# Kernel optimization log

Measured on AMD Instinct MI355X. Metric: run time of the kernel, lower is better.

## Reference

```python
import jax, jax.numpy as jnp
import numpy as np

B, F, D = 512, 128, 1024
EPS = 1e-5

def _ln(x, g, b):
    mu = jnp.mean(x, axis=-1, keepdims=True)
    var = jnp.mean(jnp.square(x - mu), axis=-1, keepdims=True)
    return (x - mu) * jax.lax.rsqrt(var + EPS) * g + b

def setup_inputs() -> dict:
    key = jax.random.key(0)
    ks = jax.random.split(key, 8)
    inp = {
        "text_embeds": jax.random.normal(ks[0], (B, D), jnp.float32),
        "video_embeds": jax.random.normal(ks[1], (B, F, D), jnp.float32),
    }
    # Linear weights: torch init is eye for all proj/linear layers; use small random
    # perturbation of identity to keep math non-trivial but realistic.
    def w(k):
        return jnp.eye(D, dtype=jnp.float32) + 0.02 * jax.random.normal(k, (D, D), jnp.float32)
    inp["q_w"], inp["k_w"], inp["v_w"] = w(ks[2]), w(ks[3]), w(ks[4])
    inp["out_w"], inp["lin_w"] = w(ks[5]), w(ks[6])
    for n in ("q_b", "k_b", "v_b", "out_b", "lin_b"):
        inp[n] = jnp.zeros((D,), jnp.float32)
    for i in (1, 2, 3):
        inp[f"ln{i}_g"] = jnp.ones((D,), jnp.float32)
        inp[f"ln{i}_b"] = jnp.zeros((D,), jnp.float32)
    return inp

def reference(text_embeds, video_embeds, q_w, k_w, v_w, out_w, lin_w,
              q_b, k_b, v_b, out_b, lin_b,
              ln1_g, ln1_b, ln2_g, ln2_b, ln3_g, ln3_b):
    t = _ln(text_embeds, ln1_g, ln1_b)                 # [B, D]
    vf = _ln(video_embeds, ln1_g, ln1_b)               # [B, F, D]
    q = t @ q_w.T + q_b                                # [B, D]
    k = vf @ k_w.T + k_b                               # [B, F, D]
    v = vf @ v_w.T + v_b                               # [B, F, D]
    logits = jnp.einsum("bd,bfd->bf", q, k) / jnp.sqrt(jnp.float32(D))
    w_att = jax.nn.softmax(logits, axis=-1)            # [B, F]
    attn = jnp.einsum("bf,bfd->bd", w_att, v)          # [B, D]
    attn = attn @ out_w.T + out_b
    attn_out = _ln(attn, ln2_g, ln2_b)
    linear_out = attn_out @ lin_w.T + lin_b
    # dropout: eval mode (identity)
    out = attn_out + linear_out
    return _ln(out, ln3_g, ln3_b)
```

## Files before the change

### kernel.cpp

```cpp
#include <hip/hip_runtime.h>

#define B_ 512
#define F_ 128
#define D_ 1024
#define EPS_ 1e-5f

typedef float f32x4 __attribute__((ext_vector_type(4)));
typedef __bf16 bf16x4 __attribute__((ext_vector_type(4)));
typedef __bf16 bf16x8 __attribute__((ext_vector_type(8)));

template <int OUT>
__global__ __launch_bounds__(256) void k_ln(
    const float* __restrict__ X, const float* __restrict__ g,
    const float* __restrict__ bv, float* __restrict__ Yf,
    __bf16* __restrict__ Yh, __bf16* __restrict__ Yl) {
  int row = blockIdx.x, t = threadIdx.x;
  f32x4 xv = *(const f32x4*)(X + (size_t)row * D_ + t * 4);
  float s = xv[0] + xv[1] + xv[2] + xv[3];
  float ss = xv[0] * xv[0] + xv[1] * xv[1] + xv[2] * xv[2] + xv[3] * xv[3];
#pragma unroll
  for (int o = 32; o > 0; o >>= 1) { s += __shfl_xor(s, o); ss += __shfl_xor(ss, o); }
  __shared__ float ws[4][2];
  int w = t >> 6;
  if ((t & 63) == 0) { ws[w][0] = s; ws[w][1] = ss; }
  __syncthreads();
  s = ws[0][0] + ws[1][0] + ws[2][0] + ws[3][0];
  ss = ws[0][1] + ws[1][1] + ws[2][1] + ws[3][1];
  float mu = s * (1.0f / D_);
  float var = ss * (1.0f / D_) - mu * mu;
  float rs = rsqrtf(var + EPS_);
  f32x4 gg = *(const f32x4*)(g + t * 4);
  f32x4 bb = *(const f32x4*)(bv + t * 4);
  f32x4 o4;
#pragma unroll
  for (int i = 0; i < 4; i++) o4[i] = (xv[i] - mu) * rs * gg[i] + bb[i];
  if (OUT == 0) {
    *(f32x4*)(Yf + (size_t)row * D_ + t * 4) = o4;
  } else {
    bf16x4 h4, l4;
#pragma unroll
    for (int i = 0; i < 4; i++) {
      h4[i] = (__bf16)o4[i];
      l4[i] = (__bf16)(o4[i] - (float)h4[i]);
    }
    *(bf16x4*)(Yh + (size_t)row * D_ + t * 4) = h4;
    *(bf16x4*)(Yl + (size_t)row * D_ + t * 4) = l4;
  }
}

__global__ __launch_bounds__(256) void k_final(
    const __bf16* __restrict__ X1h, const __bf16* __restrict__ X1l,
    const float* __restrict__ X2, const float* __restrict__ g,
    const float* __restrict__ bv, float* __restrict__ out) {
  int row = blockIdx.x, t = threadIdx.x;
  bf16x4 h4 = *(const bf16x4*)(X1h + (size_t)row * D_ + t * 4);
  bf16x4 l4 = *(const bf16x4*)(X1l + (size_t)row * D_ + t * 4);
  f32x4 b = *(const f32x4*)(X2 + (size_t)row * D_ + t * 4);
  f32x4 v;
#pragma unroll
  for (int i = 0; i < 4; i++) v[i] = (float)h4[i] + (float)l4[i] + b[i];
  float s = v[0] + v[1] + v[2] + v[3];
  float ss = v[0] * v[0] + v[1] * v[1] + v[2] * v[2] + v[3] * v[3];
#pragma unroll
  for (int o = 32; o > 0; o >>= 1) { s += __shfl_xor(s, o); ss += __shfl_xor(ss, o); }
  __shared__ float ws[4][2];
  int w = t >> 6;
  if ((t & 63) == 0) { ws[w][0] = s; ws[w][1] = ss; }
  __syncthreads();
  s = ws[0][0] + ws[1][0] + ws[2][0] + ws[3][0];
  ss = ws[0][1] + ws[1][1] + ws[2][1] + ws[3][1];
  float mu = s * (1.0f / D_);
  float var = ss * (1.0f / D_) - mu * mu;
  float rs = rsqrtf(var + EPS_);
  f32x4 gg = *(const f32x4*)(g + t * 4);
  f32x4 bb = *(const f32x4*)(bv + t * 4);
  f32x4 o4;
#pragma unroll
  for (int i = 0; i < 4; i++) o4[i] = (v[i] - mu) * rs * gg[i] + bb[i];
  *(f32x4*)(out + (size_t)row * D_ + t * 4) = o4;
}

__global__ __launch_bounds__(256) void k_wprep(
    const float* __restrict__ w0, const float* __restrict__ w1,
    const float* __restrict__ w2, const float* __restrict__ w3,
    const float* __restrict__ w4, __bf16* __restrict__ o0,
    __bf16* __restrict__ o1, __bf16* __restrict__ o2,
    __bf16* __restrict__ o3, __bf16* __restrict__ o4p,
    const float* __restrict__ text, const float* __restrict__ g1,
    const float* __restrict__ b1, __bf16* __restrict__ Yh,
    __bf16* __restrict__ Yl) {
  int z = blockIdx.z;
  int t = threadIdx.x;
  if (z == 5) {
    int row = blockIdx.y * 32 + blockIdx.x;
    if (row >= B_) return;
    f32x4 xv = *(const f32x4*)(text + (size_t)row * D_ + t * 4);
    float s = xv[0] + xv[1] + xv[2] + xv[3];
    float ss = xv[0]*xv[0] + xv[1]*xv[1] + xv[2]*xv[2] + xv[3]*xv[3];
#pragma unroll
    for (int o = 32; o > 0; o >>= 1) { s += __shfl_xor(s, o); ss += __shfl_xor(ss, o); }
    __shared__ float ws[4][2];
    int w = t >> 6;
    if ((t & 63) == 0) { ws[w][0] = s; ws[w][1] = ss; }
    __syncthreads();
    s = ws[0][0] + ws[1][0] + ws[2][0] + ws[3][0];
    ss = ws[0][1] + ws[1][1] + ws[2][1] + ws[3][1];
    float mu = s * (1.0f / D_);
    float var = ss * (1.0f / D_) - mu * mu;
    float rs = rsqrtf(var + EPS_);
    f32x4 gg = *(const f32x4*)(g1 + t * 4);
    f32x4 bb = *(const f32x4*)(b1 + t * 4);
    bf16x4 h4, l4;
#pragma unroll
    for (int i = 0; i < 4; i++) {
      float o = (xv[i] - mu) * rs * gg[i] + bb[i];
      h4[i] = (__bf16)o;
      l4[i] = (__bf16)(o - (float)h4[i]);
    }
    *(bf16x4*)(Yh + (size_t)row * D_ + t * 4) = h4;
    *(bf16x4*)(Yl + (size_t)row * D_ + t * 4) = l4;
    return;
  }
  const float* src = (z == 0) ? w0 : (z == 1) ? w1 : (z == 2) ? w2 : (z == 3) ? w3 : w4;
  __bf16* dst = (z == 0) ? o0 : (z == 1) ? o1 : (z == 2) ? o2 : (z == 3) ? o3 : o4p;
  if (z != 1) {
    int row = blockIdx.y * 32 + (t >> 3);
    int col = blockIdx.x * 32 + (t & 7) * 4;
    f32x4 v = *(const f32x4*)(src + (size_t)row * D_ + col);
    bf16x4 o;
    o[0] = (__bf16)v[0]; o[1] = (__bf16)v[1]; o[2] = (__bf16)v[2]; o[3] = (__bf16)v[3];
    *(bf16x4*)(dst + (size_t)row * D_ + col) = o;
  } else {
    __shared__ float tile[32][33];
    int ti = blockIdx.y, tj = blockIdx.x;
    int c = t & 31, r0 = t >> 5;
#pragma unroll
    for (int i = 0; i < 4; i++) {
      int r = r0 + i * 8;
      tile[r][c] = src[(size_t)(ti * 32 + r) * D_ + tj * 32 + c];
    }
    __syncthreads();
#pragma unroll
    for (int i = 0; i < 4; i++) {
      int r = r0 + i * 8;
      dst[(size_t)(tj * 32 + r) * D_ + ti * 32 + c] = (__bf16)tile[c][r];
    }
  }
}

template <int OUT>
__global__ __launch_bounds__(512) void k_gemm32(
    const __bf16* __restrict__ Ah, const __bf16* __restrict__ Al,
    const __bf16* __restrict__ W, const float* __restrict__ bias,
    float* __restrict__ Cf, __bf16* __restrict__ Ch, __bf16* __restrict__ Cl,
    int N, int K) {
  int t = threadIdx.x;
  int lane = t & 63, wv = t >> 6;
  int r = lane & 15, quad = lane >> 4;
  int tn = blockIdx.x, tm = blockIdx.y;
  int kw = K >> 3;
  const __bf16* pah0 = Ah + (size_t)(tm * 32 + r) * K + wv * kw + quad * 8;
  const __bf16* pah1 = pah0 + (size_t)16 * K;
  const __bf16* pal0 = Al + (size_t)(tm * 32 + r) * K + wv * kw + quad * 8;
  const __bf16* pal1 = pal0 + (size_t)16 * K;
  const __bf16* pw0 = W + (size_t)(tn * 32 + r) * K + wv * kw + quad * 8;
  const __bf16* pw1 = pw0 + (size_t)16 * K;
  f32x4 acc00 = {0,0,0,0}, acc01 = {0,0,0,0}, acc10 = {0,0,0,0}, acc11 = {0,0,0,0};
  bf16x8 ah0 = *(const bf16x8*)pah0, ah1 = *(const bf16x8*)pah1;
  bf16x8 al0 = *(const bf16x8*)pal0, al1 = *(const bf16x8*)pal1;
  bf16x8 w0v = *(const bf16x8*)pw0, w1v = *(const bf16x8*)pw1;
  for (int k0 = 0; k0 < kw; k0 += 32) {
    int kn = (k0 + 32 < kw) ? (k0 + 32) : 0;
    bf16x8 nah0 = *(const bf16x8*)(pah0 + kn);
    bf16x8 nah1 = *(const bf16x8*)(pah1 + kn);
    bf16x8 nal0 = *(const bf16x8*)(pal0 + kn);
    bf16x8 nal1 = *(const bf16x8*)(pal1 + kn);
    bf16x8 nw0 = *(const bf16x8*)(pw0 + kn);
    bf16x8 nw1 = *(const bf16x8*)(pw1 + kn);
    acc00 = __builtin_amdgcn_mfma_f32_16x16x32_bf16(ah0, w0v, acc00, 0, 0, 0);
    acc01 = __builtin_amdgcn_mfma_f32_16x16x32_bf16(ah0, w1v, acc01, 0, 0, 0);
    acc10 = __builtin_amdgcn_mfma_f32_16x16x32_bf16(ah1, w0v, acc10, 0, 0, 0);
    acc11 = __builtin_amdgcn_mfma_f32_16x16x32_bf16(ah1, w1v, acc11, 0, 0, 0);
    acc00 = __builtin_amdgcn_mfma_f32_16x16x32_bf16(al0, w0v, acc00, 0, 0, 0);
    acc01 = __builtin_amdgcn_mfma_f32_16x16x32_bf16(al0, w1v, acc01, 0, 0, 0);
    acc10 = __builtin_amdgcn_mfma_f32_16x16x32_bf16(al1, w0v, acc10, 0, 0, 0);
    acc11 = __builtin_amdgcn_mfma_f32_16x16x32_bf16(al1, w1v, acc11, 0, 0, 0);
    ah0 = nah0; ah1 = nah1; al0 = nal0; al1 = nal1; w0v = nw0; w1v = nw1;
  }
  __shared__ float red[8][64][17];
  *(f32x4*)(&red[wv][lane][0])  = acc00;
  *(f32x4*)(&red[wv][lane][4])  = acc01;
  *(f32x4*)(&red[wv][lane][8])  = acc10;
  *(f32x4*)(&red[wv][lane][12]) = acc11;
  __syncthreads();
  int re = lane & 15, qe = lane >> 4;
#pragma unroll
  for (int u = 0; u < 2; u++) {
    int j = (t >> 6) * 2 + u;
    int a = j >> 2, i = j & 3;
    float val = 0.0f;
#pragma unroll
    for (int ww = 0; ww < 8; ww++) val += red[ww][lane][j];
    int row = tm * 32 + qe * 4 + i + ((a >> 1) << 4);
    int col = tn * 32 + re + ((a & 1) << 4);
    if (bias) val += bias[col];
    size_t o = (size_t)row * N + col;
    if (OUT == 0) {
      Cf[o] = val;
    } else {
      __bf16 h = (__bf16)val;
      Ch[o] = h;
      Cl[o] = (__bf16)(val - (float)h);
    }
  }
}

__global__ __launch_bounds__(1024) void k_attn(
    const float* __restrict__ video, const float* __restrict__ q2,
    const __bf16* __restrict__ qh, const __bf16* __restrict__ ql,
    const float* __restrict__ g, const float* __restrict__ bv,
    const float* __restrict__ kb, __bf16* __restrict__ ctxh,
    __bf16* __restrict__ ctxl) {
  __shared__ float Xc[16][1032];
  __shared__ float mSC[16][4];
  int b = blockIdx.x, t = threadIdx.x;
  int w = t >> 6, lane = t & 63;
  const float* vbase = video + ((size_t)b * F_ + w * 8) * D_ + lane * 4;
  f32x4 vA[4], vB[4];
#pragma unroll
  for (int i = 0; i < 4; i++) vA[i] = *(const f32x4*)(vbase + i * 256);
  const float* q2p = q2 + (size_t)b * D_ + lane * 4;
  const float* gp = g + lane * 4;
  const float* bp = bv + lane * 4;
  const float* kp = kb + lane * 4;
  const __bf16* qhp = qh + (size_t)b * D_ + lane * 4;
  const __bf16* qlp = ql + (size_t)b * D_ + lane * 4;
  f32x4 gqr[4];
  float s1 = 0.f, s2 = 0.f, s3 = 0.f;
#pragma unroll
  for (int i = 0; i < 4; i++) {
    f32x4 qv = *(const f32x4*)(q2p + i * 256);
    f32x4 g4 = *(const f32x4*)(gp + i * 256);
    f32x4 b4 = *(const f32x4*)(bp + i * 256);
    f32x4 k4 = *(const f32x4*)(kp + i * 256);
    bf16x4 h4 = *(const bf16x4*)(qhp + i * 256);
    bf16x4 l4 = *(const bf16x4*)(qlp + i * 256);
#pragma unroll
    for (int j = 0; j < 4; j++) {
      float gq = g4[j] * qv[j];
      gqr[i][j] = gq;
      s1 += gq;
      s2 += b4[j] * qv[j];
      s3 += k4[j] * ((float)h4[j] + (float)l4[j]);
    }
  }
#pragma unroll
  for (int o = 32; o > 0; o >>= 1) {
    s1 += __shfl_xor(s1, o); s2 += __shfl_xor(s2, o); s3 += __shfl_xor(s3, o);
  }
  float sgq = s1, dbq = s2, qk = s3;
  f32x4 O[4];
#pragma unroll
  for (int i = 0; i < 4; i++) O[i] = (f32x4){0.f, 0.f, 0.f, 0.f};
  float m_run = -1e30f, S = 0.0f, Cc = 0.0f;
  for (int f = 0; f < 8; f++) {
    if (f < 7) {
      const float* nb = vbase + (size_t)(f + 1) * D_;
#pragma unroll
      for (int i = 0; i < 4; i++) vB[i] = *(const f32x4*)(nb + i * 256);
    }
    float sx = 0.f, sxx = 0.f, sxg = 0.f;
#pragma unroll
    for (int i = 0; i < 4; i++) {
      f32x4 v = vA[i], gg = gqr[i];
#pragma unroll
      for (int j = 0; j < 4; j++) {
        sx += v[j];
        sxx += v[j] * v[j];
        sxg += v[j] * gg[j];
      }
    }
#pragma unroll
    for (int o = 32; o > 0; o >>= 1) {
      sx += __shfl_xor(sx, o);
      sxx += __shfl_xor(sxx, o);
      sxg += __shfl_xor(sxg, o);
    }
    float mu = sx * (1.0f / D_);
    float var = sxx * (1.0f / D_) - mu * mu;
    float rs = rsqrtf(var + EPS_);
    float l = (rs * (sxg - mu * sgq) + dbq + qk) * 0.03125f;
    float m_new = fmaxf(m_run, l);
    float alpha = __expf(m_run - m_new);
    float e = __expf(l - m_new);
    float af = e * rs;
    S = S * alpha + e;
    Cc = Cc * alpha + af * mu;
#pragma unroll
    for (int i = 0; i < 4; i++) {
#pragma unroll
      for (int j = 0; j < 4; j++) O[i][j] = O[i][j] * alpha + af * vA[i][j];
    }
    m_run = m_new;
#pragma unroll
    for (int i = 0; i < 4; i++) vA[i] = vB[i];
  }
  if (lane == 0) { mSC[w][0] = m_run; mSC[w][1] = S; mSC[w][2] = Cc; }
  __syncthreads();
  float mstar = -1e30f;
#pragma unroll
  for (int i = 0; i < 16; i++) mstar = fmaxf(mstar, mSC[i][0]);
  float myscale = __expf(m_run - mstar);
#pragma unroll
  for (int i = 0; i < 4; i++) {
    f32x4 o4;
#pragma unroll
    for (int j = 0; j < 4; j++) o4[j] = O[i][j] * myscale;
    *(f32x4*)(&Xc[w][lane * 4 + i * 256]) = o4;
  }
  float Sstar = 0.f, Cstar = 0.f;
#pragma unroll
  for (int i = 0; i < 16; i++) {
    float e = __expf(mSC[i][0] - mstar);
    Sstar += mSC[i][1] * e;
    Cstar += mSC[i][2] * e;
  }
  __syncthreads();
  float Osum = 0.f;
#pragma unroll
  for (int i = 0; i < 16; i++) Osum += Xc[i][t];
  float inv = 1.0f / Sstar;
  float v = g[t] * ((Osum - Cstar) * inv) + bv[t];
  __bf16 h = (__bf16)v;
  ctxh[(size_t)b * D_ + t] = h;
  ctxl[(size_t)b * D_ + t] = (__bf16)(v - (float)h);
}

extern "C" void kernel_launch(void* const* d_in, const int* in_sizes, int n_in,
                              void* d_out, int out_size, void* d_ws, size_t ws_size,
                              hipStream_t stream) {
  (void)in_sizes; (void)n_in; (void)out_size; (void)ws_size;
  const float* text = (const float*)d_in[0];
  const float* video = (const float*)d_in[1];
  const float* q_w = (const float*)d_in[2];
  const float* k_w = (const float*)d_in[3];
  const float* v_w = (const float*)d_in[4];
  const float* out_w = (const float*)d_in[5];
  const float* lin_w = (const float*)d_in[6];
  const float* q_b = (const float*)d_in[7];
  const float* k_b = (const float*)d_in[8];
  const float* v_b = (const float*)d_in[9];
  const float* out_b = (const float*)d_in[10];
  const float* lin_b = (const float*)d_in[11];
  const float* ln1_g = (const float*)d_in[12];
  const float* ln1_b = (const float*)d_in[13];
  const float* ln2_g = (const float*)d_in[14];
  const float* ln2_b = (const float*)d_in[15];
  const float* ln3_g = (const float*)d_in[16];
  const float* ln3_b = (const float*)d_in[17];
  float* out = (float*)d_out;

  const size_t BD = (size_t)B_ * D_;
  const size_t DD = (size_t)D_ * D_;
  float* f = (float*)d_ws;
  float* slotF1 = f;
  float* slotF2 = f + BD;
  float* sum_gq = f + 2 * BD;
  __bf16* P1h = (__bf16*)(sum_gq + 4 * B_);
  __bf16* P1l = P1h + BD;
  __bf16* P2h = P1h + 2 * BD;
  __bf16* P2l = P1h + 3 * BD;
  __bf16* P3h = P1h + 4 * BD;
  __bf16* P3l = P1h + 5 * BD;
  __bf16* Wq = P1h + 6 * BD;
  __bf16* WkT = Wq + DD;
  __bf16* Wv = Wq + 2 * DD;
  __bf16* Wo = Wq + 3 * DD;
  __bf16* Wl = Wq + 4 * DD;

  dim3 gemm_grid(D_ / 32, B_ / 32);

  k_wprep<<<dim3(32, 32, 6), 256, 0, stream>>>(q_w, k_w, v_w, out_w, lin_w,
                                               Wq, WkT, Wv, Wo, Wl,
                                               text, ln1_g, ln1_b, P1h, P1l);
  k_gemm32<1><<<gemm_grid, 512, 0, stream>>>(P1h, P1l, Wq, q_b, nullptr, P2h, P2l, D_, D_);
  k_gemm32<0><<<gemm_grid, 512, 0, stream>>>(P2h, P2l, WkT, nullptr, slotF1, nullptr, nullptr, D_, D_);
  k_attn<<<B_, 1024, 0, stream>>>(video, slotF1, P2h, P2l,
                                  ln1_g, ln1_b, k_b, P1h, P1l);
  k_gemm32<1><<<gemm_grid, 512, 0, stream>>>(P1h, P1l, Wv, v_b, nullptr, P2h, P2l, D_, D_);
  k_gemm32<0><<<gemm_grid, 512, 0, stream>>>(P2h, P2l, Wo, out_b, slotF1, nullptr, nullptr, D_, D_);
  k_ln<1><<<B_, 256, 0, stream>>>(slotF1, ln2_g, ln2_b, nullptr, P3h, P3l);
  k_gemm32<0><<<gemm_grid, 512, 0, stream>>>(P3h, P3l, Wl, lin_b, slotF2, nullptr, nullptr, D_, D_);
  k_final<<<B_, 256, 0, stream>>>(P3h, P3l, slotF2, ln3_g, ln3_b, out);
}
```

Baseline: 478.8 us.

## Fuse LN2 into the final linear GEMM prologue and into the final LN kernel

Removes the standalone LN2 kernel that wrote hi/lo bf16 split activations. The linear GEMM now reads fp32 attention output, computes per-row mean and variance in its prologue, normalizes, and splits into hi/lo bf16 in registers before the MFMAs. The final kernel recomputes LN2 from fp32 before adding the linear output and applying LN3. This saves one launch and the P3 round trip, but every GEMM tile (32 column tiles per row) re-reads and re-reduces its full 1024-wide fp32 rows, so A-side traffic and reduction work are duplicated.

```diff
diff --git a/kernel.cpp b/kernel.cpp
--- a/kernel.cpp
+++ b/kernel.cpp
@@ -9,19 +9,40 @@
 typedef __bf16 bf16x4 __attribute__((ext_vector_type(4)));
 typedef __bf16 bf16x8 __attribute__((ext_vector_type(8)));
 
-template <int OUT>
-__global__ __launch_bounds__(256) void k_ln(
-    const float* __restrict__ X, const float* __restrict__ g,
-    const float* __restrict__ bv, float* __restrict__ Yf,
-    __bf16* __restrict__ Yh, __bf16* __restrict__ Yl) {
+__global__ __launch_bounds__(256) void k_final(
+    const float* __restrict__ A2, const float* __restrict__ X2,
+    const float* __restrict__ g2, const float* __restrict__ b2,
+    const float* __restrict__ g3, const float* __restrict__ b3,
+    float* __restrict__ out) {
   int row = blockIdx.x, t = threadIdx.x;
-  f32x4 xv = *(const f32x4*)(X + (size_t)row * D_ + t * 4);
-  float s = xv[0] + xv[1] + xv[2] + xv[3];
-  float ss = xv[0] * xv[0] + xv[1] * xv[1] + xv[2] * xv[2] + xv[3] * xv[3];
+  f32x4 a = *(const f32x4*)(A2 + (size_t)row * D_ + t * 4);
+  float s = a[0] + a[1] + a[2] + a[3];
+  float ss = a[0] * a[0] + a[1] * a[1] + a[2] * a[2] + a[3] * a[3];
 #pragma unroll
   for (int o = 32; o > 0; o >>= 1) { s += __shfl_xor(s, o); ss += __shfl_xor(ss, o); }
   __shared__ float ws[4][2];
   int w = t >> 6;
+  if ((t & 63) == 0) { ws[w][0] = s; ws[w][1] = ss; }
+  __syncthreads();
+  s = ws[0][0] + ws[1][0] + ws[2][0] + ws[3][0];
+  ss = ws[0][1] + ws[1][1] + ws[2][1] + ws[3][1];
+  float mu2 = s * (1.0f / D_);
+  float var2 = ss * (1.0f / D_) - mu2 * mu2;
+  float rs2 = rsqrtf(var2 + EPS_);
+  f32x4 g2v = *(const f32x4*)(g2 + t * 4);
+  f32x4 b2v = *(const f32x4*)(b2 + t * 4);
+  f32x4 lin = *(const f32x4*)(X2 + (size_t)row * D_ + t * 4);
+  f32x4 v;
+#pragma unroll
+  for (int i = 0; i < 4; i++) {
+    float attno = (a[i] - mu2) * rs2 * g2v[i] + b2v[i];
+    v[i] = attno + lin[i];
+  }
+  s = v[0] + v[1] + v[2] + v[3];
+  ss = v[0] * v[0] + v[1] * v[1] + v[2] * v[2] + v[3] * v[3];
+#pragma unroll
+  for (int o = 32; o > 0; o >>= 1) { s += __shfl_xor(s, o); ss += __shfl_xor(ss, o); }
+  __syncthreads();
   if ((t & 63) == 0) { ws[w][0] = s; ws[w][1] = ss; }
   __syncthreads();
   s = ws[0][0] + ws[1][0] + ws[2][0] + ws[3][0];
@@ -29,51 +50,8 @@
   float mu = s * (1.0f / D_);
   float var = ss * (1.0f / D_) - mu * mu;
   float rs = rsqrtf(var + EPS_);
-  f32x4 gg = *(const f32x4*)(g + t * 4);
-  f32x4 bb = *(const f32x4*)(bv + t * 4);
-  f32x4 o4;
-#pragma unroll
-  for (int i = 0; i < 4; i++) o4[i] = (xv[i] - mu) * rs * gg[i] + bb[i];
-  if (OUT == 0) {
-    *(f32x4*)(Yf + (size_t)row * D_ + t * 4) = o4;
-  } else {
-    bf16x4 h4, l4;
-#pragma unroll
-    for (int i = 0; i < 4; i++) {
-      h4[i] = (__bf16)o4[i];
-      l4[i] = (__bf16)(o4[i] - (float)h4[i]);
-    }
-    *(bf16x4*)(Yh + (size_t)row * D_ + t * 4) = h4;
-    *(bf16x4*)(Yl + (size_t)row * D_ + t * 4) = l4;
-  }
-}
-
-__global__ __launch_bounds__(256) void k_final(
-    const __bf16* __restrict__ X1h, const __bf16* __restrict__ X1l,
-    const float* __restrict__ X2, const float* __restrict__ g,
-    const float* __restrict__ bv, float* __restrict__ out) {
-  int row = blockIdx.x, t = threadIdx.x;
-  bf16x4 h4 = *(const bf16x4*)(X1h + (size_t)row * D_ + t * 4);
-  bf16x4 l4 = *(const bf16x4*)(X1l + (size_t)row * D_ + t * 4);
-  f32x4 b = *(const f32x4*)(X2 + (size_t)row * D_ + t * 4);
-  f32x4 v;
-#pragma unroll
-  for (int i = 0; i < 4; i++) v[i] = (float)h4[i] + (float)l4[i] + b[i];
-  float s = v[0] + v[1] + v[2] + v[3];
-  float ss = v[0] * v[0] + v[1] * v[1] + v[2] * v[2] + v[3] * v[3];
-#pragma unroll
-  for (int o = 32; o > 0; o >>= 1) { s += __shfl_xor(s, o); ss += __shfl_xor(ss, o); }
-  __shared__ float ws[4][2];
-  int w = t >> 6;
-  if ((t & 63) == 0) { ws[w][0] = s; ws[w][1] = ss; }
-  __syncthreads();
-  s = ws[0][0] + ws[1][0] + ws[2][0] + ws[3][0];
-  ss = ws[0][1] + ws[1][1] + ws[2][1] + ws[3][1];
-  float mu = s * (1.0f / D_);
-  float var = ss * (1.0f / D_) - mu * mu;
-  float rs = rsqrtf(var + EPS_);
-  f32x4 gg = *(const f32x4*)(g + t * 4);
-  f32x4 bb = *(const f32x4*)(bv + t * 4);
+  f32x4 gg = *(const f32x4*)(g3 + t * 4);
+  f32x4 bb = *(const f32x4*)(b3 + t * 4);
   f32x4 o4;
 #pragma unroll
   for (int i = 0; i < 4; i++) o4[i] = (v[i] - mu) * rs * gg[i] + bb[i];
@@ -215,6 +193,117 @@
   }
 }
 
+__global__ __launch_bounds__(512) void k_gemm32ln(
+    const float* __restrict__ Af, const __bf16* __restrict__ W,
+    const float* __restrict__ bias, const float* __restrict__ g2,
+    const float* __restrict__ b2, float* __restrict__ Cf, int N, int K) {
+  int t = threadIdx.x;
+  int lane = t & 63, wv = t >> 6;
+  int r = lane & 15, quad = lane >> 4;
+  int tn = blockIdx.x, tm = blockIdx.y;
+  int kw = K >> 3;
+  int kbase = wv * kw + quad * 8;
+  const float* pa0 = Af + (size_t)(tm * 32 + r) * K + kbase;
+  const float* pa1 = pa0 + (size_t)16 * K;
+  float s0 = 0.f, q0 = 0.f, s1 = 0.f, q1 = 0.f;
+#pragma unroll
+  for (int c = 0; c < 4; c++) {
+    f32x4 xa = *(const f32x4*)(pa0 + c * 32);
+    f32x4 xb = *(const f32x4*)(pa0 + c * 32 + 4);
+    f32x4 ya = *(const f32x4*)(pa1 + c * 32);
+    f32x4 yb = *(const f32x4*)(pa1 + c * 32 + 4);
+#pragma unroll
+    for (int j = 0; j < 4; j++) {
+      s0 += xa[j] + xb[j];
+      q0 += xa[j] * xa[j] + xb[j] * xb[j];
+      s1 += ya[j] + yb[j];
+      q1 += ya[j] * ya[j] + yb[j] * yb[j];
+    }
+  }
+  __shared__ float red2[2][16][2][32];
+  __shared__ float stat_s[2][32];
+  int cid = wv * 4 + quad;
+  red2[0][r][0][cid] = s0; red2[0][r][1][cid] = q0;
+  red2[1][r][0][cid] = s1; red2[1][r][1][cid] = q1;
+  __syncthreads();
+  if (t < 64) {
+    int rowid = t & 31, st = t >> 5;
+    int h = rowid >> 4, rr = rowid & 15;
+    float acc = 0.f;
+#pragma unroll
+    for (int c = 0; c < 32; c++) acc += red2[h][rr][st][c];
+    stat_s[st][rowid] = acc;
+  }
+  __syncthreads();
+  float mu0 = stat_s[0][r] * (1.0f / D_);
+  float rs0 = rsqrtf(stat_s[1][r] * (1.0f / D_) - mu0 * mu0 + EPS_);
+  float mu1 = stat_s[0][r + 16] * (1.0f / D_);
+  float rs1 = rsqrtf(stat_s[1][r + 16] * (1.0f / D_) - mu1 * mu1 + EPS_);
+  bf16x8 aH[2][4], aL[2][4];
+#pragma unroll
+  for (int c = 0; c < 4; c++) {
+    f32x4 ga = *(const f32x4*)(g2 + kbase + c * 32);
+    f32x4 gb = *(const f32x4*)(g2 + kbase + c * 32 + 4);
+    f32x4 ba = *(const f32x4*)(b2 + kbase + c * 32);
+    f32x4 bb = *(const f32x4*)(b2 + kbase + c * 32 + 4);
+    f32x4 xa = *(const f32x4*)(pa0 + c * 32);
+    f32x4 xb = *(const f32x4*)(pa0 + c * 32 + 4);
+    f32x4 ya = *(const f32x4*)(pa1 + c * 32);
+    f32x4 yb = *(const f32x4*)(pa1 + c * 32 + 4);
+    bf16x8 h0v, l0v, h1v, l1v;
+#pragma unroll
+    for (int j = 0; j < 4; j++) {
+      float o = (xa[j] - mu0) * rs0 * ga[j] + ba[j];
+      __bf16 hh = (__bf16)o; h0v[j] = hh; l0v[j] = (__bf16)(o - (float)hh);
+      o = (xb[j] - mu0) * rs0 * gb[j] + bb[j];
+      hh = (__bf16)o; h0v[4 + j] = hh; l0v[4 + j] = (__bf16)(o - (float)hh);
+      o = (ya[j] - mu1) * rs1 * ga[j] + ba[j];
+      hh = (__bf16)o; h1v[j] = hh; l1v[j] = (__bf16)(o - (float)hh);
+      o = (yb[j] - mu1) * rs1 * gb[j] + bb[j];
+      hh = (__bf16)o; h1v[4 + j] = hh; l1v[4 + j] = (__bf16)(o - (float)hh);
+    }
+    aH[0][c] = h0v; aL[0][c] = l0v; aH[1][c] = h1v; aL[1][c] = l1v;
+  }
+  const __bf16* pw0 = W + (size_t)(tn * 32 + r) * K + kbase;
+  const __bf16* pw1 = pw0 + (size_t)16 * K;
+  f32x4 acc00 = {0,0,0,0}, acc01 = {0,0,0,0}, acc10 = {0,0,0,0}, acc11 = {0,0,0,0};
+  bf16x8 w0v = *(const bf16x8*)pw0, w1v = *(const bf16x8*)pw1;
+#pragma unroll
+  for (int c = 0; c < 4; c++) {
+    int nc = (c < 3) ? (c + 1) * 32 : 0;
+    bf16x8 nw0 = *(const bf16x8*)(pw0 + nc);
+    bf16x8 nw1 = *(const bf16x8*)(pw1 + nc);
+    acc00 = __builtin_amdgcn_mfma_f32_16x16x32_bf16(aH[0][c], w0v, acc00, 0, 0, 0);
+    acc01 = __builtin_amdgcn_mfma_f32_16x16x32_bf16(aH[0][c], w1v, acc01, 0, 0, 0);
+    acc10 = __builtin_amdgcn_mfma_f32_16x16x32_bf16(aH[1][c], w0v, acc10, 0, 0, 0);
+    acc11 = __builtin_amdgcn_mfma_f32_16x16x32_bf16(aH[1][c], w1v, acc11, 0, 0, 0);
+    acc00 = __builtin_amdgcn_mfma_f32_16x16x32_bf16(aL[0][c], w0v, acc00, 0, 0, 0);
+    acc01 = __builtin_amdgcn_mfma_f32_16x16x32_bf16(aL[0][c], w1v, acc01, 0, 0, 0);
+    acc10 = __builtin_amdgcn_mfma_f32_16x16x32_bf16(aL[1][c], w0v, acc10, 0, 0, 0);
+    acc11 = __builtin_amdgcn_mfma_f32_16x16x32_bf16(aL[1][c], w1v, acc11, 0, 0, 0);
+    w0v = nw0; w1v = nw1;
+  }
+  __shared__ float red[8][64][17];
+  *(f32x4*)(&red[wv][lane][0])  = acc00;
+  *(f32x4*)(&red[wv][lane][4])  = acc01;
+  *(f32x4*)(&red[wv][lane][8])  = acc10;
+  *(f32x4*)(&red[wv][lane][12]) = acc11;
+  __syncthreads();
+  int re = lane & 15, qe = lane >> 4;
+#pragma unroll
+  for (int u = 0; u < 2; u++) {
+    int j = (t >> 6) * 2 + u;
+    int a = j >> 2, i = j & 3;
+    float val = 0.0f;
+#pragma unroll
+    for (int ww = 0; ww < 8; ww++) val += red[ww][lane][j];
+    int row = tm * 32 + qe * 4 + i + ((a >> 1) << 4);
+    int col = tn * 32 + re + ((a & 1) << 4);
+    val += bias[col];
+    Cf[(size_t)row * N + col] = val;
+  }
+}
+
 __global__ __launch_bounds__(1024) void k_attn(
     const float* __restrict__ video, const float* __restrict__ q2,
     const __bf16* __restrict__ qh, const __bf16* __restrict__ ql,
@@ -365,13 +454,11 @@
   float* f = (float*)d_ws;
   float* slotF1 = f;
   float* slotF2 = f + BD;
-  float* sum_gq = f + 2 * BD;
-  __bf16* P1h = (__bf16*)(sum_gq + 4 * B_);
+  float* scratch = f + 2 * BD;
+  __bf16* P1h = (__bf16*)(scratch + 4 * B_);
   __bf16* P1l = P1h + BD;
   __bf16* P2h = P1h + 2 * BD;
   __bf16* P2l = P1h + 3 * BD;
-  __bf16* P3h = P1h + 4 * BD;
-  __bf16* P3l = P1h + 5 * BD;
   __bf16* Wq = P1h + 6 * BD;
   __bf16* WkT = Wq + DD;
   __bf16* Wv = Wq + 2 * DD;
@@ -389,7 +476,7 @@
                                   ln1_g, ln1_b, k_b, P1h, P1l);
   k_gemm32<1><<<gemm_grid, 512, 0, stream>>>(P1h, P1l, Wv, v_b, nullptr, P2h, P2l, D_, D_);
   k_gemm32<0><<<gemm_grid, 512, 0, stream>>>(P2h, P2l, Wo, out_b, slotF1, nullptr, nullptr, D_, D_);
-  k_ln<1><<<B_, 256, 0, stream>>>(slotF1, ln2_g, ln2_b, nullptr, P3h, P3l);
-  k_gemm32<0><<<gemm_grid, 512, 0, stream>>>(P3h, P3l, Wl, lin_b, slotF2, nullptr, nullptr, D_, D_);
-  k_final<<<B_, 256, 0, stream>>>(P3h, P3l, slotF2, ln3_g, ln3_b, out);
-}
+  k_gemm32ln<<<gemm_grid, 512, 0, stream>>>(slotF1, Wl, lin_b, ln2_g, ln2_b,
+                                            slotF2, D_, D_);
+  k_final<<<B_, 256, 0, stream>>>(slotF1, slotF2, ln2_g, ln2_b, ln3_g, ln3_b, out);
+}
```

After: 483.8 us. Within noise of the previous version (+1.1%).
